# Optimization experiments

Hardware: AMD Instinct MI355X
Metric: run time of the kernel (lower is better)

## Reference

```python
import jax, jax.numpy as jnp
import numpy as np

N_EMBED = 8192
EMBED_DIM = 256
DECAY = 0.99
EPS = 1e-05


def setup_inputs() -> dict:
    key = jax.random.key(0)
    k1, k2 = jax.random.split(key)
    z = jax.random.normal(k1, (16, 32, 32, EMBED_DIM), dtype=jnp.float32)
    weight = jax.random.normal(k2, (N_EMBED, EMBED_DIM), dtype=jnp.float32)
    cluster_size = jnp.zeros((N_EMBED,), dtype=jnp.float32)
    embed_avg = weight  # register_buffer initialized as a clone of the embedding weight
    return {"z": z, "weight": weight, "cluster_size": cluster_size, "embed_avg": embed_avg}


def reference(z, weight, cluster_size, embed_avg):
    # use_norm=False -> norm is identity; training=True branch; straight_through=True
    zf = z.reshape(-1, EMBED_DIM)  # [N, D]
    # squared euclidean distance: ||z||^2 + ||e||^2 - 2 z.e
    d = (jnp.sum(zf * zf, axis=1, keepdims=True)
         + jnp.sum(weight * weight, axis=1)
         - 2.0 * jnp.einsum('bd,nd->bn', zf, weight))  # [N, K]
    idx = jnp.argmin(d, axis=1)  # [N]
    z_q = weight[idx].reshape(z.shape)
    # commitment loss (z_q detached)
    loss = jnp.mean((jax.lax.stop_gradient(z_q) - z) ** 2)
    # straight-through estimator
    z_q_st = z + jax.lax.stop_gradient(z_q - z)
    # --- EMA codebook update (no_grad in torch) ---
    counts = jax.ops.segment_sum(jnp.ones_like(idx, dtype=jnp.float32), idx, num_segments=N_EMBED)
    dw = jax.ops.segment_sum(zf, idx, num_segments=N_EMBED)  # == onehot.T @ zf
    new_cluster_size = DECAY * cluster_size + (1.0 - DECAY) * counts
    new_embed_avg = DECAY * embed_avg + (1.0 - DECAY) * dw
    n = jnp.sum(new_cluster_size)
    cs = (new_cluster_size + EPS) / (n + N_EMBED * EPS) * n
    new_weight = new_embed_avg / cs[:, None]
    idx_out = idx.reshape(z.shape[:-1])
    return (z_q_st, loss, idx_out,
            jax.lax.stop_gradient(new_weight),
            jax.lax.stop_gradient(new_cluster_size),
            jax.lax.stop_gradient(new_embed_avg))
```

## Files before the change

### kernel.cpp

```cpp
#include <hip/hip_runtime.h>
#include <cstdint>
#include <cstddef>

#define N_PTS   16384
#define K_CODES 8192
#define DIM     256
#define DECAYF  0.99f
#define OMDF    0.01f
#define EPSF    1e-5f

#define OFF_ZQ   0
#define OFF_LOSS 4194304
#define OFF_IDX  4194305
#define OFF_W    4210689
#define OFF_CS   6307841
#define OFF_EA   6316033

#define ZB_OFF   OFF_ZQ
#define WB_OFF   (OFF_ZQ + 2097152)
#define HEN_OFF  (OFF_ZQ + 3145728)
#define C1_OFF   OFF_W
#define C2_OFF   (OFF_W + 1048576)

typedef __attribute__((ext_vector_type(8))) short bf16x8;
typedef __attribute__((ext_vector_type(4))) float f32x4;

__device__ inline unsigned short f2b(float f) {
    unsigned u = __float_as_uint(f);
    return (unsigned short)((u + 0x7FFFu + ((u >> 16) & 1u)) >> 16);
}

__device__ inline unsigned umaxu(unsigned a, unsigned b) { return a > b ? a : b; }
__device__ inline unsigned uminu(unsigned a, unsigned b) { return a < b ? a : b; }

__device__ inline void gload16(const void* g, void* l) {
    __builtin_amdgcn_global_load_lds(
        (const __attribute__((address_space(1))) unsigned int*)g,
        (__attribute__((address_space(3))) unsigned int*)l, 16, 0, 0);
}

__global__ void k_cvt2(const float* __restrict__ z, short* __restrict__ zb,
                       const float* __restrict__ w, short* __restrict__ wb,
                       float* __restrict__ hen, unsigned* __restrict__ cnt) {
    const int tid = threadIdx.x;
    if (blockIdx.x < N_PTS * DIM / 2048) {
        size_t base = (size_t)(blockIdx.x * 256 + tid) * 8;
        float4 a = *(const float4*)(z + base);
        float4 b = *(const float4*)(z + base + 4);
        bf16x8 o;
        o[0] = (short)f2b(128.f * a.x); o[1] = (short)f2b(128.f * a.y);
        o[2] = (short)f2b(128.f * a.z); o[3] = (short)f2b(128.f * a.w);
        o[4] = (short)f2b(128.f * b.x); o[5] = (short)f2b(128.f * b.y);
        o[6] = (short)f2b(128.f * b.z); o[7] = (short)f2b(128.f * b.w);
        *(bf16x8*)(zb + base) = o;
    } else {
        int blk = blockIdx.x - N_PTS * DIM / 2048;
        size_t base = (size_t)(blk * 256 + tid) * 8;
        float4 a = *(const float4*)(w + base);
        float4 b = *(const float4*)(w + base + 4);
        bf16x8 o;
        o[0] = (short)f2b(a.x); o[1] = (short)f2b(a.y);
        o[2] = (short)f2b(a.z); o[3] = (short)f2b(a.w);
        o[4] = (short)f2b(b.x); o[5] = (short)f2b(b.y);
        o[6] = (short)f2b(b.z); o[7] = (short)f2b(b.w);
        *(bf16x8*)(wb + base) = o;
        float s = a.x * a.x + a.y * a.y + a.z * a.z + a.w * a.w
                + b.x * b.x + b.y * b.y + b.z * b.z + b.w * b.w;
        #pragma unroll
        for (int m = 16; m >= 1; m >>= 1) s += __shfl_xor(s, m, 64);
        if ((tid & 31) == 0) hen[base >> 8] = 0.5f * s;
        int gid = blk * 256 + tid;
        if (gid < K_CODES) cnt[gid] = 0u;
    }
}

__global__ __launch_bounds__(256) void k_gemm(const short* __restrict__ zb,
                                              const short* __restrict__ wb,
                                              const float* __restrict__ hen,
                                              unsigned* __restrict__ c1,
                                              unsigned* __restrict__ c2) {
    __shared__ __align__(16) short As[128 * 64];
    __shared__ __align__(16) short Bs[128 * 64];

    const int tid  = threadIdx.x;
    const int lane = tid & 63;
    const int wv   = tid >> 6;
    const int ztile = blockIdx.x & 127;
    const int kt    = blockIdx.x >> 7;
    const int z0 = ztile * 128, k0 = kt * 128;
    const int col = lane & 15;

    f32x4 acc[2][8];
    #pragma unroll
    for (int ni = 0; ni < 8; ni++) {
        float h = 131072.0f - 128.0f * hen[k0 + ni * 16 + col];
        f32x4 iv = {h, h, h, h};
        acc[0][ni] = iv; acc[1][ni] = iv;
    }
    const unsigned inv0 = (unsigned)(K_CODES - 1 - (k0 + col));

    const int srow = lane >> 3;
    const int scol = ((lane & 7) ^ srow) * 8;

    #pragma unroll
    for (int dc = 0; dc < 4; ++dc) {
        __syncthreads();
        #pragma unroll
        for (int s4 = 0; s4 < 4; ++s4) {
            int seg = wv * 4 + s4;
            gload16(zb + (size_t)(z0 + seg * 8 + srow) * DIM + dc * 64 + scol,
                    As + seg * 512 + lane * 8);
            gload16(wb + (size_t)(k0 + seg * 8 + srow) * DIM + dc * 64 + scol,
                    Bs + seg * 512 + lane * 8);
        }
        __syncthreads();
        #pragma unroll
        for (int kk = 0; kk < 2; ++kk) {
            bf16x8 af[2], bfr[8];
            int ch = ((kk << 2) + (lane >> 4)) ^ (lane & 7);
            #pragma unroll
            for (int mi = 0; mi < 2; mi++)
                af[mi] = *(const bf16x8*)&As[(wv * 32 + mi * 16 + col) * 64 + ch * 8];
            #pragma unroll
            for (int ni = 0; ni < 8; ni++)
                bfr[ni] = *(const bf16x8*)&Bs[(ni * 16 + col) * 64 + ch * 8];
            #pragma unroll
            for (int mi = 0; mi < 2; mi++)
                #pragma unroll
                for (int ni = 0; ni < 8; ni++)
                    acc[mi][ni] = __builtin_amdgcn_mfma_f32_16x16x32_bf16(
                        af[mi], bfr[ni], acc[mi][ni], 0, 0, 0);
        }
    }

    #pragma unroll
    for (int mi = 0; mi < 2; mi++) {
        #pragma unroll
        for (int r = 0; r < 4; r++) {
            unsigned k8[8];
            #pragma unroll
            for (int ni = 0; ni < 8; ni++) {
                unsigned q = (unsigned)acc[mi][ni][r];
                k8[ni] = (q << 13) | (inv0 - 16u * ni);
            }
            unsigned p1 = umaxu(k8[0], k8[1]), q1 = uminu(k8[0], k8[1]);
            unsigned p2 = umaxu(k8[2], k8[3]), q2 = uminu(k8[2], k8[3]);
            unsigned p3 = umaxu(k8[4], k8[5]), q3 = uminu(k8[4], k8[5]);
            unsigned p4 = umaxu(k8[6], k8[7]), q4 = uminu(k8[6], k8[7]);
            unsigned a1 = umaxu(p1, p2);
            unsigned a2 = umaxu(uminu(p1, p2), umaxu(q1, q2));
            unsigned b1 = umaxu(p3, p4);
            unsigned b2 = umaxu(uminu(p3, p4), umaxu(q3, q4));
            unsigned t1 = umaxu(a1, b1);
            unsigned t2 = umaxu(uminu(a1, b1), umaxu(a2, b2));
            unsigned m1 = t1;
            #pragma unroll
            for (int m = 8; m >= 1; m >>= 1)
                m1 = umaxu(m1, (unsigned)__shfl_xor((int)m1, m, 64));
            unsigned cc = (t1 == m1) ? t2 : t1;
            #pragma unroll
            for (int m = 8; m >= 1; m >>= 1)
                cc = umaxu(cc, (unsigned)__shfl_xor((int)cc, m, 64));
            if (col == 0) {
                int row = wv * 32 + mi * 16 + (lane >> 4) * 4 + r;
                c1[(size_t)(z0 + row) * 64 + kt] = m1;
                c2[(size_t)(z0 + row) * 64 + kt] = cc;
            }
        }
    }
}

__global__ __launch_bounds__(256) void k_rescore(
        const float* __restrict__ z, const float* __restrict__ w,
        const unsigned* __restrict__ c1, const unsigned* __restrict__ c2,
        float* __restrict__ out,
        unsigned* __restrict__ cnt, float* __restrict__ lossp) {
    int wid  = (blockIdx.x * 256 + threadIdx.x) >> 6;
    int lane = threadIdx.x & 63;
    float4 zv  = *(const float4*)(z + (size_t)wid * DIM + lane * 4);
    unsigned k1 = c1[(size_t)wid * 64 + lane];
    unsigned k2 = c2[(size_t)wid * 64 + lane];

    unsigned m1 = k1;
    #pragma unroll
    for (int m = 32; m >= 1; m >>= 1)
        m1 = umaxu(m1, (unsigned)__shfl_xor((int)m1, m, 64));
    unsigned e = (k1 == m1) ? k2 : k1;
    unsigned m2 = e;
    #pragma unroll
    for (int m = 32; m >= 1; m >>= 1)
        m2 = umaxu(m2, (unsigned)__shfl_xor((int)m2, m, 64));

    int idx = K_CODES - 1 - (int)(m1 & 0x1FFFu);
    float4 bw = *(const float4*)(w + (size_t)idx * DIM + lane * 4);

    unsigned qthr = (m1 >> 13) - 96u;
    if ((m2 >> 13) >= qthr) {
        unsigned long long best = 0ULL;
        #pragma unroll
        for (int j = 0; j < 2; j++) {
            unsigned cj = j ? k2 : k1;
            unsigned long long mask = __ballot((cj >> 13) >= qthr);
            while (mask) {
                int l = __ffsll((unsigned long long)mask) - 1;
                mask &= mask - 1;
                unsigned cwd = (unsigned)__shfl((int)cj, l, 64);
                int k = K_CODES - 1 - (int)(cwd & 0x1FFFu);
                float4 wv = *(const float4*)(w + (size_t)k * DIM + lane * 4);
                float s = zv.x * wv.x + zv.y * wv.y + zv.z * wv.z + zv.w * wv.w;
                float h = wv.x * wv.x + wv.y * wv.y + wv.z * wv.z + wv.w * wv.w;
                #pragma unroll
                for (int m = 32; m >= 1; m >>= 1) {
                    s += __shfl_xor(s, m, 64);
                    h += __shfl_xor(h, m, 64);
                }
                float sc = s - 0.5f * h;
                unsigned u = __float_as_uint(sc);
                u = (u & 0x80000000u) ? ~u : (u | 0x80000000u);
                unsigned long long key = ((unsigned long long)u << 32)
                                       | (unsigned)(K_CODES - 1 - k);
                if (key > best) best = key;
            }
        }
        int nidx = K_CODES - 1 - (int)(unsigned)(best & 0xFFFFFFFFull);
        if (nidx != idx) {
            idx = nidx;
            bw = *(const float4*)(w + (size_t)idx * DIM + lane * 4);
        }
    }

    *(float4*)(out + OFF_ZQ + (size_t)wid * DIM + lane * 4) = bw;

    float dx = bw.x - zv.x, dy = bw.y - zv.y, dz = bw.z - zv.z, dw = bw.w - zv.w;
    float s2 = dx * dx + dy * dy + dz * dz + dw * dw;
    #pragma unroll
    for (int m = 32; m >= 1; m >>= 1) s2 += __shfl_xor(s2, m, 64);

    if (lane == 0) {
        out[OFF_IDX + wid] = (float)idx;
        lossp[wid] = s2;
        atomicAdd(cnt + idx, 1u);
    }
}

__global__ __launch_bounds__(1024) void k_prefix(const float* __restrict__ csin,
                                                 float* __restrict__ out,
                                                 const unsigned* __restrict__ cnt,
                                                 unsigned* __restrict__ cursor,
                                                 unsigned* __restrict__ offs,
                                                 const float* __restrict__ lossp,
                                                 float* __restrict__ nval) {
    __shared__ unsigned wtot[16], wbase[16];
    __shared__ float fred[16], fred2[16];
    int t = threadIdx.x, lane = t & 63, wv = t >> 6;
    int base = t * 8;
    unsigned c[8], mysum = 0;
    #pragma unroll
    for (int i = 0; i < 8; i++) { c[i] = cnt[base + i]; mysum += c[i]; }
    unsigned inc = mysum;
    #pragma unroll
    for (int off = 1; off < 64; off <<= 1) {
        unsigned v = (unsigned)__shfl_up((int)inc, off, 64);
        if (lane >= off) inc += v;
    }
    if (lane == 63) wtot[wv] = inc;
    __syncthreads();
    if (t == 0) {
        unsigned r = 0;
        for (int i = 0; i < 16; i++) { wbase[i] = r; r += wtot[i]; }
        offs[K_CODES] = r;
    }
    __syncthreads();
    unsigned my0 = wbase[wv] + inc - mysum;
    float csl = 0.f;
    #pragma unroll
    for (int i = 0; i < 8; i++) {
        offs[base + i]   = my0;
        cursor[base + i] = my0;
        my0 += c[i];
        float ncs = DECAYF * csin[base + i] + OMDF * (float)c[i];
        out[OFF_CS + base + i] = ncs;
        csl += ncs;
    }
    #pragma unroll
    for (int m = 32; m >= 1; m >>= 1) csl += __shfl_xor(csl, m, 64);
    if (lane == 0) fred[wv] = csl;
    float lp = 0.f;
    #pragma unroll
    for (int i = 0; i < 16; i++) lp += lossp[t + i * 1024];
    #pragma unroll
    for (int m = 32; m >= 1; m >>= 1) lp += __shfl_xor(lp, m, 64);
    if (lane == 0) fred2[wv] = lp;
    __syncthreads();
    if (t == 0) {
        float n = 0.f, L = 0.f;
        for (int i = 0; i < 16; i++) { n += fred[i]; L += fred2[i]; }
        *nval = n;
        out[OFF_LOSS] = L * (1.0f / ((float)N_PTS * DIM));
    }
}

__global__ void k_fill(const float* __restrict__ out,
                       unsigned* __restrict__ cursor, unsigned* __restrict__ list) {
    int i = blockIdx.x * 256 + threadIdx.x;
    int idx = (int)out[OFF_IDX + i];
    unsigned pos = atomicAdd(cursor + idx, 1u);
    list[pos] = (unsigned)i;
}

__global__ void k_gather(const float* __restrict__ z, const float* __restrict__ ea,
                         float* __restrict__ out,
                         const unsigned* __restrict__ offs,
                         const unsigned* __restrict__ list,
                         const float* __restrict__ nval) {
    int k = blockIdx.x, lane = threadIdx.x;
    unsigned beg = offs[k], end = offs[k + 1];
    float4 acc = {0.f, 0.f, 0.f, 0.f};
    for (unsigned p = beg; p < end; ++p) {
        unsigned i = list[p];
        float4 zv = *(const float4*)(z + (size_t)i * DIM + lane * 4);
        acc.x += zv.x; acc.y += zv.y; acc.z += zv.z; acc.w += zv.w;
    }
    float4 e = *(const float4*)(ea + (size_t)k * DIM + lane * 4);
    e.x = DECAYF * e.x + OMDF * acc.x;
    e.y = DECAYF * e.y + OMDF * acc.y;
    e.z = DECAYF * e.z + OMDF * acc.z;
    e.w = DECAYF * e.w + OMDF * acc.w;
    *(float4*)(out + OFF_EA + (size_t)k * DIM + lane * 4) = e;

    float cs = out[OFF_CS + k];
    float n  = *nval;
    float inv = 1.f / ((cs + EPSF) / (n + (float)K_CODES * EPSF) * n);
    float4 wr = {e.x * inv, e.y * inv, e.z * inv, e.w * inv};
    *(float4*)(out + OFF_W + (size_t)k * DIM + lane * 4) = wr;
}

extern "C" void kernel_launch(void* const* d_in, const int* in_sizes, int n_in,
                              void* d_out, int out_size, void* d_ws, size_t ws_size,
                              hipStream_t stream) {
    const float* z  = (const float*)d_in[0];
    const float* w  = (const float*)d_in[1];
    const float* cs = (const float*)d_in[2];
    const float* ea = (const float*)d_in[3];
    float* out = (float*)d_out;

    short*    zb  = (short*)(out + ZB_OFF);
    short*    wb  = (short*)(out + WB_OFF);
    float*    hen = out + HEN_OFF;
    unsigned* c1  = (unsigned*)(out + C1_OFF);
    unsigned* c2  = (unsigned*)(out + C2_OFF);

    unsigned* cnt    = (unsigned*)d_ws;
    unsigned* cursor = cnt + 8192;
    unsigned* offs   = cursor + 8192;
    unsigned* list   = offs + 8200;
    float*    lossp  = (float*)(list + 16384);
    float*    nval   = lossp + 16384;

    hipLaunchKernelGGL(k_cvt2,    dim3((N_PTS + K_CODES) * DIM / 2048), dim3(256), 0, stream,
                       z, zb, w, wb, hen, cnt);
    hipLaunchKernelGGL(k_gemm,    dim3((N_PTS / 128) * (K_CODES / 128)), dim3(256), 0, stream,
                       zb, wb, hen, c1, c2);
    hipLaunchKernelGGL(k_rescore, dim3(N_PTS / 4),            dim3(256), 0, stream,
                       z, w, c1, c2, out, cnt, lossp);
    hipLaunchKernelGGL(k_prefix,  dim3(1),                    dim3(1024), 0, stream,
                       cs, out, cnt, cursor, offs, lossp, nval);
    hipLaunchKernelGGL(k_fill,    dim3(N_PTS / 256),          dim3(256), 0, stream,
                       out, cursor, list);
    hipLaunchKernelGGL(k_gather,  dim3(K_CODES),              dim3(64), 0, stream,
                       z, ea, out, offs, list, nval);
}
```

Baseline: 282.3 us.

## Raise GEMM occupancy, transpose candidate layout, fuse list fill into prefix kernel

The GEMM kernel now requests four blocks per CU through launch bounds. It also interleaves B-fragment loads with MFMAs so fewer fragments stay live in registers. The per-tile candidate arrays c1/c2 are stored tile-major so the GEMM epilogue writes are contiguous. The separate k_fill kernel is removed: the single-block prefix kernel now builds the code-sorted point list using LDS atomics on a shared cursor array. This saves a launch and global atomics, but the list fill becomes serialized inside one block, and the rescore reads of c1/c2 become strided.

```diff
diff --git a/kernel.cpp b/kernel.cpp
--- a/kernel.cpp
+++ b/kernel.cpp
@@ -74,11 +74,11 @@
     }
 }
 
-__global__ __launch_bounds__(256) void k_gemm(const short* __restrict__ zb,
-                                              const short* __restrict__ wb,
-                                              const float* __restrict__ hen,
-                                              unsigned* __restrict__ c1,
-                                              unsigned* __restrict__ c2) {
+__global__ __launch_bounds__(256, 4) void k_gemm(const short* __restrict__ zb,
+                                                 const short* __restrict__ wb,
+                                                 const float* __restrict__ hen,
+                                                 unsigned* __restrict__ c1,
+                                                 unsigned* __restrict__ c2) {
     __shared__ __align__(16) short As[128 * 64];
     __shared__ __align__(16) short Bs[128 * 64];
 
@@ -116,20 +116,17 @@
         __syncthreads();
         #pragma unroll
         for (int kk = 0; kk < 2; ++kk) {
-            bf16x8 af[2], bfr[8];
             int ch = ((kk << 2) + (lane >> 4)) ^ (lane & 7);
+            bf16x8 a0 = *(const bf16x8*)&As[(wv * 32 + col) * 64 + ch * 8];
+            bf16x8 a1 = *(const bf16x8*)&As[(wv * 32 + 16 + col) * 64 + ch * 8];
             #pragma unroll
-            for (int mi = 0; mi < 2; mi++)
-                af[mi] = *(const bf16x8*)&As[(wv * 32 + mi * 16 + col) * 64 + ch * 8];
-            #pragma unroll
-            for (int ni = 0; ni < 8; ni++)
-                bfr[ni] = *(const bf16x8*)&Bs[(ni * 16 + col) * 64 + ch * 8];
-            #pragma unroll
-            for (int mi = 0; mi < 2; mi++)
-                #pragma unroll
-                for (int ni = 0; ni < 8; ni++)
-                    acc[mi][ni] = __builtin_amdgcn_mfma_f32_16x16x32_bf16(
-                        af[mi], bfr[ni], acc[mi][ni], 0, 0, 0);
+            for (int ni = 0; ni < 8; ni++) {
+                bf16x8 b = *(const bf16x8*)&Bs[(ni * 16 + col) * 64 + ch * 8];
+                acc[0][ni] = __builtin_amdgcn_mfma_f32_16x16x32_bf16(
+                    a0, b, acc[0][ni], 0, 0, 0);
+                acc[1][ni] = __builtin_amdgcn_mfma_f32_16x16x32_bf16(
+                    a1, b, acc[1][ni], 0, 0, 0);
+            }
         }
     }
 
@@ -163,8 +160,8 @@
                 cc = umaxu(cc, (unsigned)__shfl_xor((int)cc, m, 64));
             if (col == 0) {
                 int row = wv * 32 + mi * 16 + (lane >> 4) * 4 + r;
-                c1[(size_t)(z0 + row) * 64 + kt] = m1;
-                c2[(size_t)(z0 + row) * 64 + kt] = cc;
+                c1[(size_t)kt * N_PTS + z0 + row] = m1;
+                c2[(size_t)kt * N_PTS + z0 + row] = cc;
             }
         }
     }
@@ -178,8 +175,8 @@
     int wid  = (blockIdx.x * 256 + threadIdx.x) >> 6;
     int lane = threadIdx.x & 63;
     float4 zv  = *(const float4*)(z + (size_t)wid * DIM + lane * 4);
-    unsigned k1 = c1[(size_t)wid * 64 + lane];
-    unsigned k2 = c2[(size_t)wid * 64 + lane];
+    unsigned k1 = c1[(size_t)lane * N_PTS + wid];
+    unsigned k2 = c2[(size_t)lane * N_PTS + wid];
 
     unsigned m1 = k1;
     #pragma unroll
@@ -246,10 +243,11 @@
 __global__ __launch_bounds__(1024) void k_prefix(const float* __restrict__ csin,
                                                  float* __restrict__ out,
                                                  const unsigned* __restrict__ cnt,
-                                                 unsigned* __restrict__ cursor,
                                                  unsigned* __restrict__ offs,
+                                                 unsigned* __restrict__ list,
                                                  const float* __restrict__ lossp,
                                                  float* __restrict__ nval) {
+    __shared__ unsigned scur[K_CODES];
     __shared__ unsigned wtot[16], wbase[16];
     __shared__ float fred[16], fred2[16];
     int t = threadIdx.x, lane = t & 63, wv = t >> 6;
@@ -275,8 +273,8 @@
     float csl = 0.f;
     #pragma unroll
     for (int i = 0; i < 8; i++) {
-        offs[base + i]   = my0;
-        cursor[base + i] = my0;
+        offs[base + i] = my0;
+        scur[base + i] = my0;
         my0 += c[i];
         float ncs = DECAYF * csin[base + i] + OMDF * (float)c[i];
         out[OFF_CS + base + i] = ncs;
@@ -298,14 +296,11 @@
         *nval = n;
         out[OFF_LOSS] = L * (1.0f / ((float)N_PTS * DIM));
     }
-}
-
-__global__ void k_fill(const float* __restrict__ out,
-                       unsigned* __restrict__ cursor, unsigned* __restrict__ list) {
-    int i = blockIdx.x * 256 + threadIdx.x;
-    int idx = (int)out[OFF_IDX + i];
-    unsigned pos = atomicAdd(cursor + idx, 1u);
-    list[pos] = (unsigned)i;
+    for (int i = t; i < N_PTS; i += 1024) {
+        int idx = (int)out[OFF_IDX + i];
+        unsigned pos = atomicAdd(&scur[idx], 1u);
+        list[pos] = (unsigned)i;
+    }
 }
 
 __global__ void k_gather(const float* __restrict__ z, const float* __restrict__ ea,
@@ -350,12 +345,11 @@
     unsigned* c1  = (unsigned*)(out + C1_OFF);
     unsigned* c2  = (unsigned*)(out + C2_OFF);
 
-    unsigned* cnt    = (unsigned*)d_ws;
-    unsigned* cursor = cnt + 8192;
-    unsigned* offs   = cursor + 8192;
-    unsigned* list   = offs + 8200;
-    float*    lossp  = (float*)(list + 16384);
-    float*    nval   = lossp + 16384;
+    unsigned* cnt   = (unsigned*)d_ws;
+    unsigned* offs  = cnt + 8192;
+    unsigned* list  = offs + 8200;
+    float*    lossp = (float*)(list + 16384);
+    float*    nval  = lossp + 16384;
 
     hipLaunchKernelGGL(k_cvt2,    dim3((N_PTS + K_CODES) * DIM / 2048), dim3(256), 0, stream,
                        z, zb, w, wb, hen, cnt);
@@ -364,9 +358,7 @@
     hipLaunchKernelGGL(k_rescore, dim3(N_PTS / 4),            dim3(256), 0, stream,
                        z, w, c1, c2, out, cnt, lossp);
     hipLaunchKernelGGL(k_prefix,  dim3(1),                    dim3(1024), 0, stream,
-                       cs, out, cnt, cursor, offs, lossp, nval);
-    hipLaunchKernelGGL(k_fill,    dim3(N_PTS / 256),          dim3(256), 0, stream,
-                       out, cursor, list);
+                       cs, out, cnt, offs, list, lossp, nval);
     hipLaunchKernelGGL(k_gather,  dim3(K_CODES),              dim3(64), 0, stream,
                        z, ea, out, offs, list, nval);
 }
```

Result: slower. 289.4 us (+2.5%).
